# Optimization experiments

Measured on AMD Instinct MI355X. Metric: run time of the kernel, lower is better.

The kernel has to match this reference:

```python
import jax, jax.numpy as jnp
import numpy as np

N_NODES = 100000
N_EDGES = 1600000
N_GRAPHS = 64
IN_DIM = 128
EMB_DIM = 128


def setup_inputs() -> dict:
    key = jax.random.key(0)
    ks = jax.random.split(key, 12)
    node_type = jax.random.randint(ks[0], (N_NODES,), 0, 4)
    num_inverted_predecessors = jax.random.randint(ks[1], (N_NODES,), 0, 3)
    edge_index = jax.random.randint(ks[2], (2, N_EDGES), 0, N_NODES)
    batch = jnp.sort(jax.random.randint(ks[3], (N_NODES,), 0, N_GRAPHS))
    emb_type = jax.random.normal(ks[4], (4, IN_DIM), dtype=jnp.float32) * 0.1
    emb_inv = jax.random.normal(ks[5], (3, IN_DIM), dtype=jnp.float32) * 0.1
    W0 = jax.random.normal(ks[6], (IN_DIM, EMB_DIM), dtype=jnp.float32) * 0.05
    b0 = jnp.zeros((EMB_DIM,), dtype=jnp.float32)
    W1 = jax.random.normal(ks[7], (EMB_DIM, EMB_DIM), dtype=jnp.float32) * 0.05
    b1 = jnp.zeros((EMB_DIM,), dtype=jnp.float32)
    W2 = jax.random.normal(ks[8], (EMB_DIM, EMB_DIM), dtype=jnp.float32) * 0.05
    b2 = jnpes = jnp.zeros((EMB_DIM,), dtype=jnp.float32)
    return {
        'node_type': node_type,
        'num_inverted_predecessors': num_inverted_predecessors,
        'edge_index': edge_index,
        'batch': batch,
        'emb_type': emb_type,
        'emb_inv': emb_inv,
        'W0': W0, 'b0': b0,
        'W1': W1, 'b1': b1,
        'W2': W2, 'b2': jnp.zeros((EMB_DIM,), dtype=jnp.float32),
    }


def gcn_conv(h, W, b, src, dst, n_nodes):
    # PyG GCNConv: out = D^{-1/2} (A + I) D^{-1/2} (X W) + b, all edge weights 1.
    xw = h @ W  # [N, out]
    ones = jnp.ones(dst.shape[0], dtype=h.dtype)
    deg = jax.ops.segment_sum(ones, dst, num_segments=n_nodes) + 1.0  # +1 self loop
    dinv = jax.lax.rsqrt(deg)  # deg >= 1
    coef = (dinv[dst] * dinv[src])[:, None]  # [E, 1]
    agg = jax.ops.segment_sum(xw[src] * coef, dst, num_segments=n_nodes)
    agg = agg + xw * (dinv * dinv)[:, None]  # self-loop term
    return agg + b


def reference(node_type, num_inverted_predecessors, edge_index, batch,
              emb_type, emb_inv, W0, b0, W1, b1, W2, b2):
    src, dst = edge_index[0], edge_index[1]
    n_nodes = node_type.shape[0]
    # node encoder: sum of two categorical embeddings
    h = emb_type[node_type] + emb_inv[num_inverted_predecessors]  # [N, IN_DIM]
    # layer 0, 1 with ReLU (norms are constructed but unused in the torch forward)
    h = jax.nn.relu(gcn_conv(h, W0, b0, src, dst, n_nodes))
    h = jax.nn.relu(gcn_conv(h, W1, b1, src, dst, n_nodes))
    # final layer, no activation
    h = gcn_conv(h, W2, b2, src, dst, n_nodes)
    # global readouts over batch index: max and sum
    gmax = jax.ops.segment_max(h, batch, num_segments=N_GRAPHS)
    gsum = jax.ops.segment_sum(h, batch, num_segments=N_GRAPHS)
    out = jnp.concatenate([gmax, gsum], axis=1)  # [B, 2*EMB_DIM]
    return jnp.round(out * 1000.0) / 1000.0  # torch.round(..., decimals=3)
```

## Files before the change

### kernel.cpp

```cpp
#include <hip/hip_runtime.h>
#include <hip/hip_bf16.h>
#include <cstdint>

#define NNODES 100000
#define NEDGES 1600000
#define NGRAPHS 64
#define DIM 128

#define NB 196
#define BSHIFT 9
#define SC_BLOCKS 200
#define SC_EPB (NEDGES / SC_BLOCKS)
#define EB_CAP 10000

typedef __attribute__((ext_vector_type(8))) short bf16x8;
typedef __attribute__((ext_vector_type(4))) float f32x4;

__device__ inline ushort f2bf(float f) {
  __hip_bfloat16 h = __float2bfloat16(f);
  return __builtin_bit_cast(ushort, h);
}
__device__ inline float bf2f(ushort u) {
  return __uint_as_float(((unsigned)u) << 16);
}
__device__ inline unsigned fkey(float f) {
  unsigned b = __float_as_uint(f);
  return (b & 0x80000000u) ? ~b : (b | 0x80000000u);
}
__device__ inline float fdecode(unsigned k) {
  unsigned b = (k & 0x80000000u) ? (k & 0x7FFFFFFFu) : ~k;
  return __uint_as_float(b);
}


__global__ __launch_bounds__(256) void hist2_kernel(const int* __restrict__ dst,
                                                    int* __restrict__ blockhist,
                                                    int* __restrict__ bhist) {
  __shared__ int bh[NB];
  int tid = threadIdx.x;
  if (tid < NB) bh[tid] = 0;
  __syncthreads();
  int base = blockIdx.x * SC_EPB;
  for (int o = tid * 4; o < SC_EPB; o += 1024) {
    int4 d4 = *(const int4*)(dst + base + o);
    atomicAdd(&bh[d4.x >> BSHIFT], 1);
    atomicAdd(&bh[d4.y >> BSHIFT], 1);
    atomicAdd(&bh[d4.z >> BSHIFT], 1);
    atomicAdd(&bh[d4.w >> BSHIFT], 1);
  }
  __syncthreads();
  if (tid < NB) {
    blockhist[blockIdx.x * NB + tid] = bh[tid];
    if (bh[tid]) atomicAdd(&bhist[tid], bh[tid]);
  }
}

__global__ __launch_bounds__(256) void scanB_kernel(const int* __restrict__ bhist,
                                                    const int* __restrict__ blockhist,
                                                    int* __restrict__ bbase,
                                                    int* __restrict__ blockbase,
                                                    int* __restrict__ offs) {
  __shared__ int gb[256];
  __shared__ int col[256];
  int tid = threadIdx.x;
  int b = blockIdx.x;
  int v = (tid < NB) ? bhist[tid] : 0;
  gb[tid] = v;
  __syncthreads();
  for (int o = 1; o < 256; o <<= 1) {
    int t = (tid >= o) ? gb[tid - o] : 0;
    __syncthreads();
    gb[tid] += t;
    __syncthreads();
  }
  int excl_b = gb[b] - bhist[b];
  int c = (tid < SC_BLOCKS) ? blockhist[tid * NB + b] : 0;
  col[tid] = c;
  __syncthreads();
  for (int o = 1; o < 256; o <<= 1) {
    int t = (tid >= o) ? col[tid - o] : 0;
    __syncthreads();
    col[tid] += t;
    __syncthreads();
  }
  if (tid < SC_BLOCKS) blockbase[tid * NB + b] = excl_b + col[tid] - c;
  if (tid == 0) {
    bbase[b] = excl_b;
    if (b == 0) { bbase[NB] = NEDGES; offs[NNODES] = NEDGES; }
  }
}

__global__ __launch_bounds__(256) void scatter2_kernel(const int* __restrict__ src,
                                                       const int* __restrict__ dst,
                                                       const int* __restrict__ blockbase,
                                                       unsigned* __restrict__ gbuf) {
  __shared__ int lcur[NB];
  int tid = threadIdx.x;
  if (tid < NB) lcur[tid] = blockbase[blockIdx.x * NB + tid];
  __syncthreads();
  int base = blockIdx.x * SC_EPB;
  for (int o = tid * 4; o < SC_EPB; o += 1024) {
    int4 s4 = *(const int4*)(src + base + o);
    int4 d4 = *(const int4*)(dst + base + o);
    int ss[4] = {s4.x, s4.y, s4.z, s4.w};
    int dd[4] = {d4.x, d4.y, d4.z, d4.w};
#pragma unroll
    for (int u = 0; u < 4; ++u) {
      int bk = dd[u] >> BSHIFT;
      unsigned rec = (unsigned)ss[u] | ((unsigned)(dd[u] & 511) << 17);
      int pos = atomicAdd(&lcur[bk], 1);
      gbuf[pos] = rec;
    }
  }
}

__global__ __launch_bounds__(256) void bucket_sort(const unsigned* __restrict__ gbuf,
                                                   const int* __restrict__ bhist,
                                                   const int* __restrict__ bbase,
                                                   int* __restrict__ csr_src,
                                                   int* __restrict__ offs,
                                                   float* __restrict__ dinv) {
  __shared__ int lhist[512];
  __shared__ int lscan[512];
  __shared__ int lcur2[512];
  __shared__ int lcsr[EB_CAP];
  int tid = threadIdx.x;
  int b = blockIdx.x;
  int ebase = bbase[b];
  int bsize = bhist[b];
  lhist[tid] = 0; lhist[tid + 256] = 0;
  lcur2[tid] = 0; lcur2[tid + 256] = 0;
  __syncthreads();
  for (int k = tid; k < bsize; k += 256)
    atomicAdd(&lhist[(gbuf[ebase + k] >> 17) & 511], 1);
  __syncthreads();
  lscan[tid] = lhist[tid];
  lscan[tid + 256] = lhist[tid + 256];
  __syncthreads();
  for (int o = 1; o < 256; o <<= 1) {
    int a = (tid >= o) ? lscan[tid - o] : 0;
    int c = (tid >= o) ? lscan[256 + tid - o] : 0;
    __syncthreads();
    lscan[tid] += a;
    lscan[256 + tid] += c;
    __syncthreads();
  }
  int tot = lscan[255];
  __syncthreads();
  lscan[256 + tid] += tot;
  __syncthreads();
  int nodebase = b << BSHIFT;
#pragma unroll
  for (int hh = 0; hh < 2; ++hh) {
    int l = hh * 256 + tid;
    int i = nodebase + l;
    if (i < NNODES) {
      int c = lhist[l];
      offs[i] = ebase + (lscan[l] - c);
      dinv[i] = rsqrtf((float)c + 1.0f);
    }
  }
  for (int k = tid; k < bsize; k += 256) {
    unsigned e = gbuf[ebase + k];
    int l = (e >> 17) & 511;
    int p = atomicAdd(&lcur2[l], 1);
    int pos = (lscan[l] - lhist[l]) + p;
    if (pos < EB_CAP) lcsr[pos] = (int)(e & 0x1FFFFu);
  }
  __syncthreads();
  for (int k = tid; k < bsize; k += 256) csr_src[ebase + k] = lcsr[k];
}


__global__ __launch_bounds__(128) void prep_kernel(const float* __restrict__ et,
                                                   const float* __restrict__ ei,
                                                   const float* __restrict__ W0,
                                                   const float* __restrict__ W1,
                                                   const float* __restrict__ W2,
                                                   float* __restrict__ TW,
                                                   ushort* __restrict__ wbf) {
  int b = blockIdx.x;
  int tid = threadIdx.x;
  if (b < 7) {
    const float* in = (b < 4) ? (et + b * DIM) : (ei + (b - 4) * DIM);
    float acc = 0.f;
    for (int k = 0; k < DIM; ++k) acc += in[k] * W0[k * DIM + tid];
    TW[b * DIM + tid] = acc;
  } else {
    int m = (b - 7) >> 4;
    int blk = (b - 7) & 15;
    const float* w = m ? W2 : W1;
    ushort* o = wbf + (size_t)m * DIM * DIM;
    int base = blk * 1024 + tid * 8;
    float4 a = *(const float4*)(w + base);
    float4 c = *(const float4*)(w + base + 4);
    uint4 r;
    r.x = ((unsigned)f2bf(a.y) << 16) | f2bf(a.x);
    r.y = ((unsigned)f2bf(a.w) << 16) | f2bf(a.z);
    r.z = ((unsigned)f2bf(c.y) << 16) | f2bf(c.x);
    r.w = ((unsigned)f2bf(c.w) << 16) | f2bf(c.z);
    *(uint4*)(o + base) = r;
  }
}


__global__ __launch_bounds__(256) void coef_kernel(const int* __restrict__ offs,
                                                   const int* __restrict__ csr_src,
                                                   const int* __restrict__ nt,
                                                   const int* __restrict__ nv,
                                                   const float* __restrict__ dinv,
                                                   float* __restrict__ Cbuf) {
  int gid = blockIdx.x * 256 + threadIdx.x;
  int i = gid >> 2;
  int sl = gid & 3;
  if (i >= NNODES) return;
  int s0 = offs[i], s1 = offs[i + 1];
  float c0 = 0.f, c1 = 0.f, c2 = 0.f, c3 = 0.f, c4 = 0.f, c5 = 0.f, c6 = 0.f;
  for (int j = s0 + sl; j < s1; j += 4) {
    int s = csr_src[j];
    float dv = dinv[s];
    int t = nt[s], v = nv[s];
    c0 += (t == 0) ? dv : 0.f;
    c1 += (t == 1) ? dv : 0.f;
    c2 += (t == 2) ? dv : 0.f;
    c3 += (t == 3) ? dv : 0.f;
    c4 += (v == 0) ? dv : 0.f;
    c5 += (v == 1) ? dv : 0.f;
    c6 += (v == 2) ? dv : 0.f;
  }
#pragma unroll
  for (int o = 1; o < 4; o <<= 1) {
    c0 += __shfl_xor(c0, o);
    c1 += __shfl_xor(c1, o);
    c2 += __shfl_xor(c2, o);
    c3 += __shfl_xor(c3, o);
    c4 += __shfl_xor(c4, o);
    c5 += __shfl_xor(c5, o);
    c6 += __shfl_xor(c6, o);
  }
  if (sl == 0) {
    float di = dinv[i];
    int t = nt[i], v = nv[i];
    c0 += (t == 0) ? di : 0.f;
    c1 += (t == 1) ? di : 0.f;
    c2 += (t == 2) ? di : 0.f;
    c3 += (t == 3) ? di : 0.f;
    c4 += (v == 0) ? di : 0.f;
    c5 += (v == 1) ? di : 0.f;
    c6 += (v == 2) ? di : 0.f;
    float4 lo = {c0, c1, c2, c3};
    float4 hi = {c4, c5, c6, 0.f};
    *(float4*)(Cbuf + (size_t)i * 8) = lo;
    *(float4*)(Cbuf + (size_t)i * 8 + 4) = hi;
  }
}

__global__ void h1_kernel(const float* __restrict__ Cbuf, const float* __restrict__ TW,
                          const float* __restrict__ dinv, const float* __restrict__ b0,
                          ushort* __restrict__ h) {
  int idx = blockIdx.x * blockDim.x + threadIdx.x;
  if (idx >= NNODES * 32) return;
  int i = idx >> 5, d4 = (idx & 31) << 2;
  const float* C = Cbuf + (size_t)i * 8;
  float4 acc = {0.f, 0.f, 0.f, 0.f};
#pragma unroll
  for (int k = 0; k < 7; ++k) {
    float ck = C[k];
    float4 tw = *(const float4*)(TW + k * DIM + d4);
    acc.x += ck * tw.x; acc.y += ck * tw.y;
    acc.z += ck * tw.z; acc.w += ck * tw.w;
  }
  float di = dinv[i];
  float4 bb = *(const float4*)(b0 + d4);
  float vx = fmaxf(di * acc.x + bb.x, 0.f);
  float vy = fmaxf(di * acc.y + bb.y, 0.f);
  float vz = fmaxf(di * acc.z + bb.z, 0.f);
  float vw = fmaxf(di * acc.w + bb.w, 0.f);
  uint2 o;
  o.x = ((unsigned)f2bf(vy) << 16) | f2bf(vx);
  o.y = ((unsigned)f2bf(vw) << 16) | f2bf(vz);
  *(uint2*)(h + (size_t)i * DIM + d4) = o;
}


__global__ __launch_bounds__(256) void gemm_kernel(const ushort* __restrict__ h,
                                                   const ushort* __restrict__ wb,
                                                   const float* __restrict__ dinv,
                                                   ushort* __restrict__ out) {
  __shared__ ushort Ws[32 * 64 * 8];
  int tid = threadIdx.x;
  for (int g = tid; g < 2048; g += 256) {
    int kt = g >> 6, l = g & 63;
    int ks = kt >> 3, t = kt & 7;
    int kb = ks * 32 + ((l >> 4) << 3);
    int col = t * 16 + (l & 15);
#pragma unroll
    for (int j = 0; j < 8; ++j) Ws[g * 8 + j] = wb[(kb + j) * DIM + col];
  }
  __syncthreads();
  int w = tid >> 6, lane = tid & 63;
  for (int tile = blockIdx.x * 4 + w; tile < NNODES / 16; tile += gridDim.x * 4) {
    int row0 = tile * 16;
    const ushort* hrow = h + (size_t)(row0 + (lane & 15)) * DIM + ((lane >> 4) << 3);
    f32x4 acc[8];
#pragma unroll
    for (int t = 0; t < 8; ++t) acc[t] = {0.f, 0.f, 0.f, 0.f};
#pragma unroll
    for (int ks = 0; ks < 4; ++ks) {
      bf16x8 a = *(const bf16x8*)(hrow + ks * 32);
#pragma unroll
      for (int t = 0; t < 8; ++t) {
        bf16x8 b = *(const bf16x8*)&Ws[((ks * 8 + t) * 64 + lane) * 8];
        acc[t] = __builtin_amdgcn_mfma_f32_16x16x32_bf16(a, b, acc[t], 0, 0, 0);
      }
    }
    int rbase = row0 + ((lane >> 4) << 2);
    int cbase = lane & 15;
    float4 dv = *(const float4*)(dinv + rbase);
    float dvr[4] = {dv.x, dv.y, dv.z, dv.w};
#pragma unroll
    for (int t = 0; t < 8; ++t)
#pragma unroll
      for (int r = 0; r < 4; ++r)
        out[(size_t)(rbase + r) * DIM + t * 16 + cbase] = f2bf(acc[t][r] * dvr[r]);
  }
}


__global__ __launch_bounds__(256, 8) void agg_kernel(const ushort* __restrict__ xws,
                                                     const int* __restrict__ offs,
                                                     const int* __restrict__ csr_src,
                                                     const float* __restrict__ dinv,
                                                     const float* __restrict__ bias,
                                                     ushort* __restrict__ outb, int relu) {
  int i = blockIdx.x * 4 + (threadIdx.x >> 6);
  if (i >= NNODES) return;
  int lane = threadIdx.x & 63;
  int s0 = offs[i], s1 = offs[i + 1];
  float ax = 0.f, ay = 0.f;
  int j = s0;
  for (; j + 16 <= s1; j += 16) {
    int s[16];
#pragma unroll
    for (int u = 0; u < 16; ++u) s[u] = csr_src[j + u];
    unsigned p[16];
#pragma unroll
    for (int u = 0; u < 16; ++u)
      p[u] = *(const unsigned*)(xws + (size_t)s[u] * DIM + lane * 2);
#pragma unroll
    for (int u = 0; u < 16; ++u) {
      ax += bf2f((ushort)(p[u] & 0xffffu));
      ay += bf2f((ushort)(p[u] >> 16));
    }
  }
  for (; j + 4 <= s1; j += 4) {
    int s[4];
#pragma unroll
    for (int u = 0; u < 4; ++u) s[u] = csr_src[j + u];
    unsigned p[4];
#pragma unroll
    for (int u = 0; u < 4; ++u)
      p[u] = *(const unsigned*)(xws + (size_t)s[u] * DIM + lane * 2);
#pragma unroll
    for (int u = 0; u < 4; ++u) {
      ax += bf2f((ushort)(p[u] & 0xffffu));
      ay += bf2f((ushort)(p[u] >> 16));
    }
  }
  for (; j < s1; ++j) {
    int sa = csr_src[j];
    unsigned pa = *(const unsigned*)(xws + (size_t)sa * DIM + lane * 2);
    ax += bf2f((ushort)(pa & 0xffffu));
    ay += bf2f((ushort)(pa >> 16));
  }
  unsigned ps = *(const unsigned*)(xws + (size_t)i * DIM + lane * 2);
  ax += bf2f((ushort)(ps & 0xffffu));
  ay += bf2f((ushort)(ps >> 16));
  float di = dinv[i];
  float2 b = *(const float2*)(bias + lane * 2);
  float vx = di * ax + b.x;
  float vy = di * ay + b.y;
  if (relu) { vx = fmaxf(vx, 0.f); vy = fmaxf(vy, 0.f); }
  *(unsigned*)(outb + (size_t)i * DIM + lane * 2) =
      ((unsigned)f2bf(vy) << 16) | f2bf(vx);
}


__global__ __launch_bounds__(128) void readout_kernel(const ushort* __restrict__ h,
                                                      const int* __restrict__ batch,
                                                      unsigned* __restrict__ gmaxk,
                                                      float* __restrict__ gsum) {
  int d = threadIdx.x;
  int start = blockIdx.x * 128;
  if (start >= NNODES) return;
  int end = min(start + 128, NNODES);
  int cur = batch[start];
  float s = 0.f, m = -INFINITY;
  for (int i = start; i < end; ++i) {
    int g = batch[i];
    float v = bf2f(h[(size_t)i * DIM + d]);
    if (g != cur) {
      atomicAdd(&gsum[cur * DIM + d], s);
      atomicMax(&gmaxk[cur * DIM + d], fkey(m));
      cur = g; s = 0.f; m = -INFINITY;
    }
    s += v;
    m = fmaxf(m, v);
  }
  atomicAdd(&gsum[cur * DIM + d], s);
  atomicMax(&gmaxk[cur * DIM + d], fkey(m));
}

__global__ void pack_kernel(const unsigned* __restrict__ gmaxk,
                            const float* __restrict__ gsum, float* __restrict__ out) {
  int idx = blockIdx.x * blockDim.x + threadIdx.x;
  if (idx >= NGRAPHS * 256) return;
  int g = idx >> 8, d = idx & 255;
  float v = (d < 128) ? fdecode(gmaxk[g * DIM + d]) : gsum[g * DIM + (d - 128)];
  out[idx] = rintf(v * 1000.0f) / 1000.0f;
}


extern "C" void kernel_launch(void* const* d_in, const int* in_sizes, int n_in,
                              void* d_out, int out_size, void* d_ws, size_t ws_size,
                              hipStream_t stream) {
  const int* node_type = (const int*)d_in[0];
  const int* ninv      = (const int*)d_in[1];
  const int* edge      = (const int*)d_in[2];
  const int* batch     = (const int*)d_in[3];
  const float* emb_type = (const float*)d_in[4];
  const float* emb_inv  = (const float*)d_in[5];
  const float* W0 = (const float*)d_in[6];
  const float* B[3] = {(const float*)d_in[7], (const float*)d_in[9], (const float*)d_in[11]};
  const float* W1 = (const float*)d_in[8];
  const float* W2 = (const float*)d_in[10];
  const int* srcp = edge;
  const int* dstp = edge + NEDGES;
  float* out = (float*)d_out;

  char* ws = (char*)d_ws;
  auto alloc = [&](size_t bytes) {
    char* p = ws;
    ws += (bytes + 255) & ~(size_t)255;
    return p;
  };
  ushort* hA     = (ushort*)alloc((size_t)NNODES * DIM * 2);
  ushort* xws    = (ushort*)alloc((size_t)NNODES * DIM * 2);
  float* dinv    = (float*)alloc((size_t)NNODES * 4);
  int* offs      = (int*)alloc((size_t)(NNODES + 1) * 4);
  int* csr_src   = (int*)alloc((size_t)NEDGES * 4);
  unsigned* gbuf = (unsigned*)alloc((size_t)NEDGES * 4);
  float* Cbuf    = (float*)alloc((size_t)NNODES * 8 * 4);
  unsigned* gmaxk = (unsigned*)alloc((size_t)NGRAPHS * DIM * 4);
  float* gsum    = (float*)alloc((size_t)NGRAPHS * DIM * 4);
  int* bhist     = (int*)alloc((size_t)NB * 4);
  int* bbase     = (int*)alloc((size_t)(NB + 1) * 4);
  int* blockhist = (int*)alloc((size_t)SC_BLOCKS * NB * 4);
  int* blockbase = (int*)alloc((size_t)SC_BLOCKS * NB * 4);
  float* TW      = (float*)alloc((size_t)7 * DIM * 4);
  ushort* wbf    = (ushort*)alloc((size_t)2 * DIM * DIM * 2);

  hipMemsetAsync(gmaxk, 0, (size_t)NGRAPHS * DIM * 4 * 2 + NB * 4, stream);

  hist2_kernel<<<SC_BLOCKS, 256, 0, stream>>>(dstp, blockhist, bhist);
  scanB_kernel<<<NB, 256, 0, stream>>>(bhist, blockhist, bbase, blockbase, offs);
  scatter2_kernel<<<SC_BLOCKS, 256, 0, stream>>>(srcp, dstp, blockbase, gbuf);
  bucket_sort<<<NB, 256, 0, stream>>>(gbuf, bhist, bbase, csr_src, offs, dinv);

  prep_kernel<<<39, 128, 0, stream>>>(emb_type, emb_inv, W0, W1, W2, TW, wbf);
  coef_kernel<<<(NNODES * 4 + 255) / 256, 256, 0, stream>>>(offs, csr_src, node_type,
                                                            ninv, dinv, Cbuf);
  h1_kernel<<<NNODES * 32 / 256, 256, 0, stream>>>(Cbuf, TW, dinv, B[0], hA);

  for (int l = 1; l < 3; ++l) {
    gemm_kernel<<<1024, 256, 0, stream>>>(hA, wbf + (size_t)(l - 1) * DIM * DIM, dinv, xws);
    agg_kernel<<<NNODES / 4, 256, 0, stream>>>(xws, offs, csr_src, dinv, B[l],
                                               hA, l < 2 ? 1 : 0);
  }

  readout_kernel<<<(NNODES + 127) / 128, 128, 0, stream>>>(hA, batch, gmaxk, gsum);
  pack_kernel<<<64, 256, 0, stream>>>(gmaxk, gsum, out);
}
```

Measured before the change: 295.4 us.

## Stage scatter in LDS, pack node attributes, fuse coef and h1 kernels

The scatter kernel now sorts each block's edges by bucket in shared memory and then writes them out, so global writes are grouped by bucket instead of going to scattered positions. Node degree-normalisation, type and inverted-count are packed into one 32-bit word per node, which cuts the three gathers per edge in the coefficient pass to one. The coefficient kernel is unrolled for more loads in flight and fused with the first-layer embedding matmul, so the Cbuf round trip and one kernel launch go away. In exchange the packed dinv loses its low 4 mantissa bits, and the scatter kernel uses a large shared-memory buffer that may lower occupancy.

```diff
diff --git a/kernel.cpp b/kernel.cpp
--- a/kernel.cpp
+++ b/kernel.cpp
@@ -90,15 +90,36 @@
   }
 }
 
-__global__ __launch_bounds__(256) void scatter2_kernel(const int* __restrict__ src,
+__global__ __launch_bounds__(256) void scatter3_kernel(const int* __restrict__ src,
                                                        const int* __restrict__ dst,
+                                                       const int* __restrict__ blockhist,
                                                        const int* __restrict__ blockbase,
                                                        unsigned* __restrict__ gbuf) {
-  __shared__ int lcur[NB];
+  __shared__ unsigned rec[SC_EPB];
+  __shared__ ushort bid[SC_EPB];
+  __shared__ int sbuf[256];
+  __shared__ int Ls[NB];
+  __shared__ int cur[NB];
+  __shared__ int Gb[NB];
   int tid = threadIdx.x;
-  if (tid < NB) lcur[tid] = blockbase[blockIdx.x * NB + tid];
-  __syncthreads();
-  int base = blockIdx.x * SC_EPB;
+  int b = blockIdx.x;
+  int c = (tid < NB) ? blockhist[b * NB + tid] : 0;
+  sbuf[tid] = c;
+  __syncthreads();
+  for (int o = 1; o < 256; o <<= 1) {
+    int t = (tid >= o) ? sbuf[tid - o] : 0;
+    __syncthreads();
+    sbuf[tid] += t;
+    __syncthreads();
+  }
+  if (tid < NB) {
+    int excl = sbuf[tid] - c;
+    Ls[tid] = excl;
+    cur[tid] = excl;
+    Gb[tid] = blockbase[b * NB + tid];
+  }
+  __syncthreads();
+  int base = b * SC_EPB;
   for (int o = tid * 4; o < SC_EPB; o += 1024) {
     int4 s4 = *(const int4*)(src + base + o);
     int4 d4 = *(const int4*)(dst + base + o);
@@ -107,19 +128,27 @@
 #pragma unroll
     for (int u = 0; u < 4; ++u) {
       int bk = dd[u] >> BSHIFT;
-      unsigned rec = (unsigned)ss[u] | ((unsigned)(dd[u] & 511) << 17);
-      int pos = atomicAdd(&lcur[bk], 1);
-      gbuf[pos] = rec;
-    }
+      int p = atomicAdd(&cur[bk], 1);
+      rec[p] = (unsigned)ss[u] | ((unsigned)(dd[u] & 511) << 17);
+      bid[p] = (ushort)bk;
+    }
+  }
+  __syncthreads();
+  for (int j = tid; j < SC_EPB; j += 256) {
+    int bk = bid[j];
+    gbuf[Gb[bk] + (j - Ls[bk])] = rec[j];
   }
 }
 
 __global__ __launch_bounds__(256) void bucket_sort(const unsigned* __restrict__ gbuf,
                                                    const int* __restrict__ bhist,
                                                    const int* __restrict__ bbase,
+                                                   const int* __restrict__ nt,
+                                                   const int* __restrict__ nv,
                                                    int* __restrict__ csr_src,
                                                    int* __restrict__ offs,
-                                                   float* __restrict__ dinv) {
+                                                   float* __restrict__ dinv,
+                                                   unsigned* __restrict__ pk) {
   __shared__ int lhist[512];
   __shared__ int lscan[512];
   __shared__ int lcur2[512];
@@ -157,7 +186,10 @@
     if (i < NNODES) {
       int c = lhist[l];
       offs[i] = ebase + (lscan[l] - c);
-      dinv[i] = rsqrtf((float)c + 1.0f);
+      float dv = rsqrtf((float)c + 1.0f);
+      dinv[i] = dv;
+      pk[i] = (__float_as_uint(dv) & 0xFFFFFFF0u) |
+              ((unsigned)nt[i] << 2) | (unsigned)nv[i];
     }
   }
   for (int k = tid; k < bsize; k += 256) {
@@ -204,30 +236,44 @@
 }
 
 
-__global__ __launch_bounds__(256) void coef_kernel(const int* __restrict__ offs,
-                                                   const int* __restrict__ csr_src,
-                                                   const int* __restrict__ nt,
-                                                   const int* __restrict__ nv,
-                                                   const float* __restrict__ dinv,
-                                                   float* __restrict__ Cbuf) {
+__device__ inline void pk_accum(unsigned p, float& c0, float& c1, float& c2, float& c3,
+                                float& c4, float& c5, float& c6) {
+  float dv = __uint_as_float(p & 0xFFFFFFF0u);
+  int t = (p >> 2) & 3, v = p & 3;
+  c0 += (t == 0) ? dv : 0.f;
+  c1 += (t == 1) ? dv : 0.f;
+  c2 += (t == 2) ? dv : 0.f;
+  c3 += (t == 3) ? dv : 0.f;
+  c4 += (v == 0) ? dv : 0.f;
+  c5 += (v == 1) ? dv : 0.f;
+  c6 += (v == 2) ? dv : 0.f;
+}
+
+__global__ __launch_bounds__(256) void coefh1_kernel(const int* __restrict__ offs,
+                                                     const int* __restrict__ csr_src,
+                                                     const unsigned* __restrict__ pk,
+                                                     const float* __restrict__ dinv,
+                                                     const float* __restrict__ TW,
+                                                     const float* __restrict__ b0,
+                                                     ushort* __restrict__ h) {
   int gid = blockIdx.x * 256 + threadIdx.x;
   int i = gid >> 2;
   int sl = gid & 3;
   if (i >= NNODES) return;
   int s0 = offs[i], s1 = offs[i + 1];
   float c0 = 0.f, c1 = 0.f, c2 = 0.f, c3 = 0.f, c4 = 0.f, c5 = 0.f, c6 = 0.f;
-  for (int j = s0 + sl; j < s1; j += 4) {
-    int s = csr_src[j];
-    float dv = dinv[s];
-    int t = nt[s], v = nv[s];
-    c0 += (t == 0) ? dv : 0.f;
-    c1 += (t == 1) ? dv : 0.f;
-    c2 += (t == 2) ? dv : 0.f;
-    c3 += (t == 3) ? dv : 0.f;
-    c4 += (v == 0) ? dv : 0.f;
-    c5 += (v == 1) ? dv : 0.f;
-    c6 += (v == 2) ? dv : 0.f;
-  }
+  int j = s0 + sl;
+  for (; j + 12 < s1; j += 16) {
+    int s_[4];
+#pragma unroll
+    for (int u = 0; u < 4; ++u) s_[u] = csr_src[j + 4 * u];
+    unsigned p_[4];
+#pragma unroll
+    for (int u = 0; u < 4; ++u) p_[u] = pk[s_[u]];
+#pragma unroll
+    for (int u = 0; u < 4; ++u) pk_accum(p_[u], c0, c1, c2, c3, c4, c5, c6);
+  }
+  for (; j < s1; j += 4) pk_accum(pk[csr_src[j]], c0, c1, c2, c3, c4, c5, c6);
 #pragma unroll
   for (int o = 1; o < 4; o <<= 1) {
     c0 += __shfl_xor(c0, o);
@@ -238,9 +284,10 @@
     c5 += __shfl_xor(c5, o);
     c6 += __shfl_xor(c6, o);
   }
-  if (sl == 0) {
-    float di = dinv[i];
-    int t = nt[i], v = nv[i];
+  float di = dinv[i];
+  {
+    unsigned pb = pk[i];
+    int t = (pb >> 2) & 3, v = pb & 3;
     c0 += (t == 0) ? di : 0.f;
     c1 += (t == 1) ? di : 0.f;
     c2 += (t == 2) ? di : 0.f;
@@ -248,38 +295,53 @@
     c4 += (v == 0) ? di : 0.f;
     c5 += (v == 1) ? di : 0.f;
     c6 += (v == 2) ? di : 0.f;
-    float4 lo = {c0, c1, c2, c3};
-    float4 hi = {c4, c5, c6, 0.f};
-    *(float4*)(Cbuf + (size_t)i * 8) = lo;
-    *(float4*)(Cbuf + (size_t)i * 8 + 4) = hi;
-  }
-}
-
-__global__ void h1_kernel(const float* __restrict__ Cbuf, const float* __restrict__ TW,
-                          const float* __restrict__ dinv, const float* __restrict__ b0,
-                          ushort* __restrict__ h) {
-  int idx = blockIdx.x * blockDim.x + threadIdx.x;
-  if (idx >= NNODES * 32) return;
-  int i = idx >> 5, d4 = (idx & 31) << 2;
-  const float* C = Cbuf + (size_t)i * 8;
-  float4 acc = {0.f, 0.f, 0.f, 0.f};
+  }
+  float cs[7] = {c0, c1, c2, c3, c4, c5, c6};
+  const float4* TW4 = (const float4*)TW;
+  f32x4 acc[8];
+#pragma unroll
+  for (int q = 0; q < 8; ++q) acc[q] = {0.f, 0.f, 0.f, 0.f};
 #pragma unroll
   for (int k = 0; k < 7; ++k) {
-    float ck = C[k];
-    float4 tw = *(const float4*)(TW + k * DIM + d4);
-    acc.x += ck * tw.x; acc.y += ck * tw.y;
-    acc.z += ck * tw.z; acc.w += ck * tw.w;
-  }
-  float di = dinv[i];
-  float4 bb = *(const float4*)(b0 + d4);
-  float vx = fmaxf(di * acc.x + bb.x, 0.f);
-  float vy = fmaxf(di * acc.y + bb.y, 0.f);
-  float vz = fmaxf(di * acc.z + bb.z, 0.f);
-  float vw = fmaxf(di * acc.w + bb.w, 0.f);
-  uint2 o;
-  o.x = ((unsigned)f2bf(vy) << 16) | f2bf(vx);
-  o.y = ((unsigned)f2bf(vw) << 16) | f2bf(vz);
-  *(uint2*)(h + (size_t)i * DIM + d4) = o;
+    float ck = cs[k];
+#pragma unroll
+    for (int q = 0; q < 8; ++q) {
+      float4 tw = TW4[k * 32 + sl * 8 + q];
+      acc[q][0] += ck * tw.x;
+      acc[q][1] += ck * tw.y;
+      acc[q][2] += ck * tw.z;
+      acc[q][3] += ck * tw.w;
+    }
+  }
+  int dbase = sl * 32;
+  uint4 o0, o1;
+  unsigned word[8];
+#pragma unroll
+  for (int q = 0; q < 8; ++q) {
+    float4 bb = *(const float4*)(b0 + dbase + q * 4);
+    float vx = fmaxf(di * acc[q][0] + bb.x, 0.f);
+    float vy = fmaxf(di * acc[q][1] + bb.y, 0.f);
+    float vz = fmaxf(di * acc[q][2] + bb.z, 0.f);
+    float vw = fmaxf(di * acc[q][3] + bb.w, 0.f);
+    word[q] = 0;
+    unsigned lo = ((unsigned)f2bf(vy) << 16) | f2bf(vx);
+    unsigned hi = ((unsigned)f2bf(vw) << 16) | f2bf(vz);
+    if (q == 0) { o0.x = lo; o0.y = hi; }
+    else if (q == 1) { o0.z = lo; o0.w = hi; }
+    else if (q == 2) { o1.x = lo; o1.y = hi; }
+    else if (q == 3) { o1.z = lo; o1.w = hi; }
+    else if (q == 4) { o0 = o0; word[0] = lo; word[1] = hi; }
+    else if (q == 5) { word[2] = lo; word[3] = hi; }
+    else if (q == 6) { word[4] = lo; word[5] = hi; }
+    else { word[6] = lo; word[7] = hi; }
+  }
+  ushort* dst = h + (size_t)i * DIM + dbase;
+  *(uint4*)(dst) = o0;
+  *(uint4*)(dst + 8) = o1;
+  uint4 o2 = {word[0], word[1], word[2], word[3]};
+  uint4 o3 = {word[4], word[5], word[6], word[7]};
+  *(uint4*)(dst + 16) = o2;
+  *(uint4*)(dst + 24) = o3;
 }
 
 
@@ -447,10 +509,10 @@
   ushort* hA     = (ushort*)alloc((size_t)NNODES * DIM * 2);
   ushort* xws    = (ushort*)alloc((size_t)NNODES * DIM * 2);
   float* dinv    = (float*)alloc((size_t)NNODES * 4);
+  unsigned* pk   = (unsigned*)alloc((size_t)NNODES * 4);
   int* offs      = (int*)alloc((size_t)(NNODES + 1) * 4);
   int* csr_src   = (int*)alloc((size_t)NEDGES * 4);
   unsigned* gbuf = (unsigned*)alloc((size_t)NEDGES * 4);
-  float* Cbuf    = (float*)alloc((size_t)NNODES * 8 * 4);
   unsigned* gmaxk = (unsigned*)alloc((size_t)NGRAPHS * DIM * 4);
   float* gsum    = (float*)alloc((size_t)NGRAPHS * DIM * 4);
   int* bhist     = (int*)alloc((size_t)NB * 4);
@@ -464,13 +526,13 @@
 
   hist2_kernel<<<SC_BLOCKS, 256, 0, stream>>>(dstp, blockhist, bhist);
   scanB_kernel<<<NB, 256, 0, stream>>>(bhist, blockhist, bbase, blockbase, offs);
-  scatter2_kernel<<<SC_BLOCKS, 256, 0, stream>>>(srcp, dstp, blockbase, gbuf);
-  bucket_sort<<<NB, 256, 0, stream>>>(gbuf, bhist, bbase, csr_src, offs, dinv);
+  scatter3_kernel<<<SC_BLOCKS, 256, 0, stream>>>(srcp, dstp, blockhist, blockbase, gbuf);
+  bucket_sort<<<NB, 256, 0, stream>>>(gbuf, bhist, bbase, node_type, ninv,
+                                      csr_src, offs, dinv, pk);
 
   prep_kernel<<<39, 128, 0, stream>>>(emb_type, emb_inv, W0, W1, W2, TW, wbf);
-  coef_kernel<<<(NNODES * 4 + 255) / 256, 256, 0, stream>>>(offs, csr_src, node_type,
-                                                            ninv, dinv, Cbuf);
-  h1_kernel<<<NNODES * 32 / 256, 256, 0, stream>>>(Cbuf, TW, dinv, B[0], hA);
+  coefh1_kernel<<<(NNODES * 4 + 255) / 256, 256, 0, stream>>>(offs, csr_src, pk, dinv,
+                                                              TW, B[0], hA);
 
   for (int l = 1; l < 3; ++l) {
     gemm_kernel<<<1024, 256, 0, stream>>>(hA, wbf + (size_t)(l - 1) * DIM * DIM, dinv, xws);
```

Measured after the change: 311.1 us. +5.3%, slower.
